# Kernel tuning notes

Hardware: AMD Instinct MI355X
Metric: run time of the kernel (lower is better)

The kernel has to match this reference:

```python
import jax, jax.numpy as jnp
import numpy as np

B, D_IN, C, P = 8192, 2048, 1000, 256


def setup_inputs() -> dict:
    key = jax.random.key(0)
    ks = jax.random.split(key, 6)
    return {
        "x": jax.random.normal(ks[0], (B, D_IN), dtype=jnp.float32),
        "Wm": jax.random.normal(ks[1], (C, D_IN), dtype=jnp.float32) * (1.0 / np.sqrt(D_IN)),
        "bm": jax.random.normal(ks[2], (C,), dtype=jnp.float32) * 0.01,
        "u": jax.random.normal(ks[3], (P, C), dtype=jnp.float32),
        "v": jax.random.normal(ks[4], (P, C), dtype=jnp.float32),
        "w": jax.random.normal(ks[5], (P, 1), dtype=jnp.float32),
    }


def reference(x, Wm, bm, u, v, w):
    # Backbone: Linear(D_IN -> C) producing per-instance logits (B, C)
    preds = jnp.einsum("bd,cd->bc", x, Wm) + bm
    # Gated attention, fully batched (replaces per-instance Python loop):
    # tanh(u @ pred) * sigmoid(v @ pred)  -> (B, P)
    gated = jnp.tanh(jnp.einsum("bc,pc->bp", preds, u)) * jax.nn.sigmoid(
        jnp.einsum("bc,pc->bp", preds, v)
    )
    scores = (gated @ w).ravel()          # (B,)
    attention = jax.nn.softmax(scores)    # softmax over instances
    total_pred = jnp.sum(preds * attention[:, None])
    return preds, total_pred
```

## Files before the change

### kernel.cpp

```cpp
#include <hip/hip_runtime.h>
#include <hip/hip_fp16.h>

typedef _Float16 half8 __attribute__((ext_vector_type(8)));
typedef float f32x4 __attribute__((ext_vector_type(4)));

#define B_   8192
#define DIN  2048
#define C_   1000
#define CP   1024
#define NP2  512

static const size_t OFF_XH  = 0;
static const size_t OFF_WH  = OFF_XH  + (size_t)B_ * DIN * 2;
static const size_t OFF_UVH = OFF_WH  + (size_t)CP * DIN * 2;
static const size_t OFF_PH  = OFF_UVH + (size_t)NP2 * CP * 2;
static const size_t OFF_SC  = OFF_PH  + (size_t)B_ * CP * 2;
static const size_t OFF_RS  = OFF_SC  + (size_t)B_ * 4;
static const size_t WS_NEED = OFF_RS  + (size_t)B_ * 4;

__device__ __forceinline__ void gload16(const void* g, void* l) {
  __builtin_amdgcn_global_load_lds(
      (const __attribute__((address_space(1))) void*)g,
      (__attribute__((address_space(3))) void*)l, 16, 0, 0);
}

__global__ __launch_bounds__(256) void prep_kernel(
    const float* __restrict__ x, const float* __restrict__ Wm,
    const float* __restrict__ u, const float* __restrict__ v,
    _Float16* __restrict__ xh, _Float16* __restrict__ wh,
    _Float16* __restrict__ uvh, float* __restrict__ scores,
    float* __restrict__ rowsum)
{
  const long NX  = (long)B_ * DIN / 8;
  const long NW  = (long)CP * DIN / 8;
  const long NUV = (long)NP2 * CP / 8;
  const long NZ  = 2 * (long)B_ / 8;
  const long T   = NX + NW + NUV + NZ;
  for (long idx = (long)blockIdx.x * blockDim.x + threadIdx.x; idx < T;
       idx += (long)gridDim.x * blockDim.x) {
    if (idx < NX) {
      long e = idx * 8;
      float4 p0 = *(const float4*)(x + e);
      float4 p1 = *(const float4*)(x + e + 4);
      half8 h;
      h[0] = (_Float16)p0.x; h[1] = (_Float16)p0.y; h[2] = (_Float16)p0.z; h[3] = (_Float16)p0.w;
      h[4] = (_Float16)p1.x; h[5] = (_Float16)p1.y; h[6] = (_Float16)p1.z; h[7] = (_Float16)p1.w;
      *(half8*)(xh + e) = h;
    } else if (idx < NX + NW) {
      long e = (idx - NX) * 8;
      int row = (int)(e >> 11);
      half8 h;
      if (row < C_) {
        float4 p0 = *(const float4*)(Wm + e);
        float4 p1 = *(const float4*)(Wm + e + 4);
        h[0] = (_Float16)p0.x; h[1] = (_Float16)p0.y; h[2] = (_Float16)p0.z; h[3] = (_Float16)p0.w;
        h[4] = (_Float16)p1.x; h[5] = (_Float16)p1.y; h[6] = (_Float16)p1.z; h[7] = (_Float16)p1.w;
      } else {
        h = (half8)(_Float16)0.f;
      }
      *(half8*)(wh + e) = h;
    } else if (idx < NX + NW + NUV) {
      long e = (idx - NX - NW) * 8;
      int j = (int)(e >> 10);
      int k = (int)(e & 1023);
      const float* src = (j & 1) ? v : u;
      int p = j >> 1;
      half8 h;
      #pragma unroll
      for (int t = 0; t < 8; ++t) {
        int kk = k + t;
        h[t] = (kk < C_) ? (_Float16)src[(size_t)p * C_ + kk] : (_Float16)0.f;
      }
      *(half8*)(uvh + e) = h;
    } else {
      long e = (idx - NX - NW - NUV) * 8;
      float4 z = {0.f, 0.f, 0.f, 0.f};
      if (e < B_) {
        *(float4*)(scores + e) = z; *(float4*)(scores + e + 4) = z;
      } else {
        long r = e - B_;
        *(float4*)(rowsum + r) = z; *(float4*)(rowsum + r + 4) = z;
      }
    }
  }
}

__global__ __launch_bounds__(512) void gemm1_kernel(
    const _Float16* __restrict__ xh, const _Float16* __restrict__ wh,
    const float* __restrict__ bmv, float* __restrict__ preds,
    _Float16* __restrict__ predsh, float* __restrict__ rowsum)
{
  __shared__ _Float16 lds[3 * 24576];
  const int tid  = threadIdx.x;
  const int lane = tid & 63;
  const int w    = tid >> 6;
  const int wm   = w >> 2;
  const int wn   = w & 3;
  const int bm0  = blockIdx.x * 256;
  const int bn0  = blockIdx.y * 128;

  f32x4 acc[8][2] = {};

  const _Float16* srcA[4];
  const _Float16* srcB[2];
  #pragma unroll
  for (int k = 0; k < 4; ++k) {
    int slot = k * 512 + tid;
    int row  = slot >> 3;
    int cb   = (slot & 7) << 4;
    int scb  = cb ^ ((row & 7) << 4);
    srcA[k] = xh + (size_t)(bm0 + row) * DIN + (scb >> 1);
  }
  #pragma unroll
  for (int k = 0; k < 2; ++k) {
    int slot = k * 512 + tid;
    int row  = slot >> 3;
    int cb   = (slot & 7) << 4;
    int scb  = cb ^ ((row & 7) << 4);
    srcB[k] = wh + (size_t)(bn0 + row) * DIN + (scb >> 1);
  }

  int aoff[8][2], boff[2][2];
  #pragma unroll
  for (int m = 0; m < 8; ++m) {
    #pragma unroll
    for (int ks = 0; ks < 2; ++ks) {
      int ra = wm * 128 + m * 16 + (lane & 15);
      int kb = ks * 64 + (lane >> 4) * 16;
      aoff[m][ks] = ra * 128 + (kb ^ ((ra & 7) << 4));
    }
  }
  #pragma unroll
  for (int n = 0; n < 2; ++n) {
    #pragma unroll
    for (int ks = 0; ks < 2; ++ks) {
      int rb = wn * 32 + n * 16 + (lane & 15);
      int kb = ks * 64 + (lane >> 4) * 16;
      boff[n][ks] = 32768 + rb * 128 + (kb ^ ((rb & 7) << 4));
    }
  }

  auto stageSet = [&](int b, int which) {
    char* base = (char*)lds + b * 49152;
    if (which < 4) gload16(srcA[which], base + which * 8192 + w * 1024);
    else           gload16(srcB[which - 4], base + 32768 + (which - 4) * 8192 + w * 1024);
  };
  auto advance = [&]() {
    #pragma unroll
    for (int k = 0; k < 4; ++k) srcA[k] += 64;
    #pragma unroll
    for (int k = 0; k < 2; ++k) srcB[k] += 64;
  };

  const int NT = DIN / 64;

  #pragma unroll
  for (int q = 0; q < 6; ++q) stageSet(0, q);
  advance();
  #pragma unroll
  for (int q = 0; q < 6; ++q) stageSet(1, q);
  advance();
  asm volatile("s_waitcnt vmcnt(6)" ::: "memory");
  __builtin_amdgcn_s_barrier();
  asm volatile("" ::: "memory");

  int c = 0;
  #pragma unroll 1
  for (int t = 0; t < NT; ++t) {
    const char* bufc = (const char*)lds + c * 49152;
    int sb = c - 1; if (sb < 0) sb = 2;
    const bool st = (t + 2 < NT);

    half8 a2[4][2], b2[2][2];
    #pragma unroll
    for (int m = 0; m < 4; ++m)
      #pragma unroll
      for (int ks = 0; ks < 2; ++ks)
        a2[m][ks] = *(const half8*)(bufc + aoff[m][ks]);
    #pragma unroll
    for (int n = 0; n < 2; ++n)
      #pragma unroll
      for (int ks = 0; ks < 2; ++ks)
        b2[n][ks] = *(const half8*)(bufc + boff[n][ks]);
    if (st) { stageSet(sb, 0); stageSet(sb, 1); stageSet(sb, 2); }
    __builtin_amdgcn_s_barrier();
    asm volatile("" ::: "memory");
    __builtin_amdgcn_s_setprio(1);
    #pragma unroll
    for (int m = 0; m < 4; ++m)
      #pragma unroll
      for (int n = 0; n < 2; ++n)
        #pragma unroll
        for (int ks = 0; ks < 2; ++ks)
          acc[m][n] = __builtin_amdgcn_mfma_f32_16x16x32_f16(a2[m][ks], b2[n][ks], acc[m][n], 0, 0, 0);
    __builtin_amdgcn_s_setprio(0);
    __builtin_amdgcn_s_barrier();
    asm volatile("" ::: "memory");

    #pragma unroll
    for (int m = 0; m < 4; ++m)
      #pragma unroll
      for (int ks = 0; ks < 2; ++ks)
        a2[m][ks] = *(const half8*)(bufc + aoff[m + 4][ks]);
    if (st) { stageSet(sb, 3); stageSet(sb, 4); stageSet(sb, 5); advance(); }
    __builtin_amdgcn_s_barrier();
    asm volatile("" ::: "memory");
    __builtin_amdgcn_s_setprio(1);
    #pragma unroll
    for (int m = 0; m < 4; ++m)
      #pragma unroll
      for (int n = 0; n < 2; ++n)
        #pragma unroll
        for (int ks = 0; ks < 2; ++ks)
          acc[m + 4][n] = __builtin_amdgcn_mfma_f32_16x16x32_f16(a2[m][ks], b2[n][ks], acc[m + 4][n], 0, 0, 0);
    __builtin_amdgcn_s_setprio(0);
    if (st)                 asm volatile("s_waitcnt vmcnt(6)" ::: "memory");
    else if (t + 1 < NT)    asm volatile("s_waitcnt vmcnt(0)" ::: "memory");
    __builtin_amdgcn_s_barrier();
    asm volatile("" ::: "memory");

    c = (c == 2) ? 0 : c + 1;
  }

  float rp[8][4] = {};
  #pragma unroll
  for (int m = 0; m < 8; ++m) {
    #pragma unroll
    for (int n = 0; n < 2; ++n) {
      f32x4 d = acc[m][n];
      int gc = bn0 + wn * 32 + n * 16 + (lane & 15);
      float bias = (gc < C_) ? bmv[gc] : 0.f;
      #pragma unroll
      for (int j = 0; j < 4; ++j) {
        int gr = bm0 + wm * 128 + m * 16 + (lane >> 4) * 4 + j;
        float val = d[j] + bias;
        predsh[(size_t)gr * CP + gc] = (_Float16)val;
        if (gc < C_) preds[(size_t)gr * C_ + gc] = val;
        rp[m][j] += val;
      }
    }
  }
  #pragma unroll
  for (int m = 0; m < 8; ++m) {
    #pragma unroll
    for (int j = 0; j < 4; ++j) {
      float s = rp[m][j];
      s += __shfl_xor(s, 1); s += __shfl_xor(s, 2);
      s += __shfl_xor(s, 4); s += __shfl_xor(s, 8);
      if ((lane & 15) == 0) {
        int gr = bm0 + wm * 128 + m * 16 + (lane >> 4) * 4 + j;
        atomicAdd(&rowsum[gr], s);
      }
    }
  }
}

__global__ __launch_bounds__(256) void gemm2_kernel(
    const _Float16* __restrict__ predsh, const _Float16* __restrict__ uvh,
    const float* __restrict__ wv, float* __restrict__ scores)
{
  __shared__ _Float16 sA[2][64 * 64];
  __shared__ _Float16 sB[2][128 * 64];
  const int tid  = threadIdx.x;
  const int lane = tid & 63;
  const int w    = tid >> 6;
  const int wm   = w >> 1, wn = w & 1;
  const int bm0  = blockIdx.x * 64;
  const int bn0  = blockIdx.y * 128;

  f32x4 acc[2][4] = {};

  const _Float16* srcA[2]; const _Float16* srcB[4];
  #pragma unroll
  for (int i = 0; i < 2; ++i) {
    int slot = i * 256 + tid;
    int row  = slot >> 3;
    int cb   = (slot & 7) << 4;
    int scb  = cb ^ ((row & 7) << 4);
    srcA[i] = predsh + (size_t)(bm0 + row) * CP + (scb >> 1);
  }
  #pragma unroll
  for (int i = 0; i < 4; ++i) {
    int slot = i * 256 + tid;
    int row  = slot >> 3;
    int cb   = (slot & 7) << 4;
    int scb  = cb ^ ((row & 7) << 4);
    srcB[i] = uvh + (size_t)(bn0 + row) * CP + (scb >> 1);
  }
  int aoff[2][2], boff[4][2];
  #pragma unroll
  for (int ks = 0; ks < 2; ++ks) {
    int kb = ks * 64 + (lane >> 4) * 16;
    #pragma unroll
    for (int mi = 0; mi < 2; ++mi) {
      int ra = wm * 32 + mi * 16 + (lane & 15);
      aoff[mi][ks] = ra * 128 + (kb ^ ((ra & 7) << 4));
    }
    #pragma unroll
    for (int ni = 0; ni < 4; ++ni) {
      int rb = wn * 64 + ni * 16 + (lane & 15);
      boff[ni][ks] = rb * 128 + (kb ^ ((rb & 7) << 4));
    }
  }

  auto stage = [&](int c) {
    #pragma unroll
    for (int i = 0; i < 2; ++i) {
      gload16(srcA[i], &sA[c][(i * 4 + w) * 512]);
      srcA[i] += 64;
    }
    #pragma unroll
    for (int i = 0; i < 4; ++i) {
      gload16(srcB[i], &sB[c][(i * 4 + w) * 512]);
      srcB[i] += 64;
    }
  };

  auto compute = [&](int c) {
    const char* bA = (const char*)&sA[c][0];
    const char* bB = (const char*)&sB[c][0];
    #pragma unroll
    for (int ks = 0; ks < 2; ++ks) {
      half8 a[2], b[4];
      #pragma unroll
      for (int mi = 0; mi < 2; ++mi) a[mi] = *(const half8*)(bA + aoff[mi][ks]);
      #pragma unroll
      for (int ni = 0; ni < 4; ++ni) b[ni] = *(const half8*)(bB + boff[ni][ks]);
      #pragma unroll
      for (int mi = 0; mi < 2; ++mi)
        #pragma unroll
        for (int ni = 0; ni < 4; ++ni)
          acc[mi][ni] = __builtin_amdgcn_mfma_f32_16x16x32_f16(a[mi], b[ni], acc[mi][ni], 0, 0, 0);
    }
  };

  const int NT = CP / 64;
  stage(0);
  #pragma unroll 1
  for (int kt = 0; kt < NT; kt += 2) {
    stage(1);
    asm volatile("s_waitcnt vmcnt(6)" ::: "memory");
    __builtin_amdgcn_s_barrier();
    asm volatile("" ::: "memory");
    compute(0);
    __builtin_amdgcn_s_barrier();
    asm volatile("" ::: "memory");
    if (kt + 2 < NT) {
      stage(0);
      asm volatile("s_waitcnt vmcnt(6)" ::: "memory");
    } else {
      asm volatile("s_waitcnt vmcnt(0)" ::: "memory");
    }
    __builtin_amdgcn_s_barrier();
    asm volatile("" ::: "memory");
    compute(1);
    __builtin_amdgcn_s_barrier();
    asm volatile("" ::: "memory");
  }

  float sp[2][4] = {};
  #pragma unroll
  for (int mi = 0; mi < 2; ++mi) {
    #pragma unroll
    for (int ni = 0; ni < 4; ++ni) {
      f32x4 d = acc[mi][ni];
      int gc = bn0 + wn * 64 + ni * 16 + (lane & 15);
      float wq = wv[gc >> 1];
      bool even = ((gc & 1) == 0);
      #pragma unroll
      for (int j = 0; j < 4; ++j) {
        float t  = d[j];
        float pr = __shfl_xor(t, 1);
        float th = 2.f / (1.f + __expf(-2.f * t)) - 1.f;
        float sg = 1.f / (1.f + __expf(-pr));
        sp[mi][j] += even ? (th * sg * wq) : 0.f;
      }
    }
  }
  #pragma unroll
  for (int mi = 0; mi < 2; ++mi) {
    #pragma unroll
    for (int j = 0; j < 4; ++j) {
      float s = sp[mi][j];
      s += __shfl_xor(s, 1); s += __shfl_xor(s, 2);
      s += __shfl_xor(s, 4); s += __shfl_xor(s, 8);
      if ((lane & 15) == 0) {
        int gr = bm0 + wm * 32 + mi * 16 + (lane >> 4) * 4 + j;
        atomicAdd(&scores[gr], s);
      }
    }
  }
}

__global__ __launch_bounds__(1024) void final_kernel(
    const float* __restrict__ scores, const float* __restrict__ rowsum,
    float* __restrict__ out)
{
  __shared__ float red[16], red2[16];
  const int t = threadIdx.x;
  const int lane = t & 63, wid = t >> 6;
  float s[8];
  float m = -3.4e38f;
  #pragma unroll
  for (int i = 0; i < 8; ++i) { s[i] = scores[t + i * 1024]; m = fmaxf(m, s[i]); }
  #pragma unroll
  for (int off = 1; off < 64; off <<= 1) m = fmaxf(m, __shfl_xor(m, off));
  if (lane == 0) red[wid] = m;
  __syncthreads();
  #pragma unroll
  for (int i = 0; i < 16; ++i) m = fmaxf(m, red[i]);
  __syncthreads();

  float se = 0.f, sr = 0.f;
  #pragma unroll
  for (int i = 0; i < 8; ++i) {
    float e = __expf(s[i] - m);
    se += e;
    sr += e * rowsum[t + i * 1024];
  }
  #pragma unroll
  for (int off = 1; off < 64; off <<= 1) { se += __shfl_xor(se, off); sr += __shfl_xor(sr, off); }
  if (lane == 0) { red[wid] = se; red2[wid] = sr; }
  __syncthreads();
  if (t == 0) {
    float tse = 0.f, tsr = 0.f;
    for (int i = 0; i < 16; ++i) { tse += red[i]; tsr += red2[i]; }
    out[0] = tsr / tse;
  }
}

extern "C" void kernel_launch(void* const* d_in, const int* in_sizes, int n_in,
                              void* d_out, int out_size, void* d_ws, size_t ws_size,
                              hipStream_t stream)
{
  const float* x   = (const float*)d_in[0];
  const float* Wm  = (const float*)d_in[1];
  const float* bmv = (const float*)d_in[2];
  const float* u   = (const float*)d_in[3];
  const float* v   = (const float*)d_in[4];
  const float* wv  = (const float*)d_in[5];
  float* out = (float*)d_out;

  if (ws_size < WS_NEED) return;

  char* ws = (char*)d_ws;
  _Float16* xh     = (_Float16*)(ws + OFF_XH);
  _Float16* wh     = (_Float16*)(ws + OFF_WH);
  _Float16* uvh    = (_Float16*)(ws + OFF_UVH);
  _Float16* predsh = (_Float16*)(ws + OFF_PH);
  float*    scores = (float*)(ws + OFF_SC);
  float*    rowsum = (float*)(ws + OFF_RS);

  prep_kernel<<<2048, 256, 0, stream>>>(x, Wm, u, v, xh, wh, uvh, scores, rowsum);
  gemm1_kernel<<<dim3(32, 8), 512, 0, stream>>>(xh, wh, bmv, out, predsh, rowsum);
  gemm2_kernel<<<dim3(128, 4), 256, 0, stream>>>(predsh, uvh, wv, scores);
  final_kernel<<<1, 1024, 0, stream>>>(scores, rowsum, out + (size_t)B_ * C_);
}
```

Baseline: 96.04 us.

## Reshape gemm1 warp tiling to 4x4 and software-pipeline LDS fragment reads across quadrants

```diff
diff --git a/kernel.cpp b/kernel.cpp
--- a/kernel.cpp
+++ b/kernel.cpp
@@ -17,6 +17,9 @@
 static const size_t OFF_SC  = OFF_PH  + (size_t)B_ * CP * 2;
 static const size_t OFF_RS  = OFF_SC  + (size_t)B_ * 4;
 static const size_t WS_NEED = OFF_RS  + (size_t)B_ * 4;
+
+#define FENCE asm volatile("" ::: "memory")
+#define BARRIER do { FENCE; __builtin_amdgcn_s_barrier(); FENCE; } while (0)
 
 __device__ __forceinline__ void gload16(const void* g, void* l) {
   __builtin_amdgcn_global_load_lds(
@@ -94,12 +97,12 @@
   const int tid  = threadIdx.x;
   const int lane = tid & 63;
   const int w    = tid >> 6;
-  const int wm   = w >> 2;
-  const int wn   = w & 3;
+  const int wm   = w >> 1;
+  const int wn   = w & 1;
   const int bm0  = blockIdx.x * 256;
   const int bn0  = blockIdx.y * 128;
 
-  f32x4 acc[8][2] = {};
+  f32x4 acc[4][4] = {};
 
   const _Float16* srcA[4];
   const _Float16* srcB[2];
@@ -120,119 +123,194 @@
     srcB[k] = wh + (size_t)(bn0 + row) * DIN + (scb >> 1);
   }
 
-  int aoff[8][2], boff[2][2];
-  #pragma unroll
-  for (int m = 0; m < 8; ++m) {
+  int aoff[4][2], boff[4][2];
+  #pragma unroll
+  for (int m = 0; m < 4; ++m) {
     #pragma unroll
     for (int ks = 0; ks < 2; ++ks) {
-      int ra = wm * 128 + m * 16 + (lane & 15);
+      int ra = wm * 64 + m * 16 + (lane & 15);
       int kb = ks * 64 + (lane >> 4) * 16;
       aoff[m][ks] = ra * 128 + (kb ^ ((ra & 7) << 4));
     }
   }
   #pragma unroll
-  for (int n = 0; n < 2; ++n) {
+  for (int n = 0; n < 4; ++n) {
     #pragma unroll
     for (int ks = 0; ks < 2; ++ks) {
-      int rb = wn * 32 + n * 16 + (lane & 15);
+      int rb = wn * 64 + n * 16 + (lane & 15);
       int kb = ks * 64 + (lane >> 4) * 16;
       boff[n][ks] = 32768 + rb * 128 + (kb ^ ((rb & 7) << 4));
     }
   }
 
-  auto stageSet = [&](int b, int which) {
-    char* base = (char*)lds + b * 49152;
-    if (which < 4) gload16(srcA[which], base + which * 8192 + w * 1024);
-    else           gload16(srcB[which - 4], base + 32768 + (which - 4) * 8192 + w * 1024);
+  half8 aLa[2][2], aLb[2][2], aHf[2][2], bLf[2][2], bHf[2][2];
+
+  auto stA = [&](int cs, int k) {
+    gload16(srcA[k], (char*)lds + cs * 49152 + k * 8192 + w * 1024);
+  };
+  auto stB = [&](int cs, int k) {
+    gload16(srcB[k], (char*)lds + cs * 49152 + 32768 + k * 8192 + w * 1024);
   };
   auto advance = [&]() {
     #pragma unroll
     for (int k = 0; k < 4; ++k) srcA[k] += 64;
-    #pragma unroll
-    for (int k = 0; k < 2; ++k) srcB[k] += 64;
-  };
-
-  const int NT = DIN / 64;
-
-  #pragma unroll
-  for (int q = 0; q < 6; ++q) stageSet(0, q);
-  advance();
-  #pragma unroll
-  for (int q = 0; q < 6; ++q) stageSet(1, q);
-  advance();
-  asm volatile("s_waitcnt vmcnt(6)" ::: "memory");
-  __builtin_amdgcn_s_barrier();
-  asm volatile("" ::: "memory");
-
-  int c = 0;
-  #pragma unroll 1
-  for (int t = 0; t < NT; ++t) {
-    const char* bufc = (const char*)lds + c * 49152;
-    int sb = c - 1; if (sb < 0) sb = 2;
-    const bool st = (t + 2 < NT);
-
-    half8 a2[4][2], b2[2][2];
-    #pragma unroll
-    for (int m = 0; m < 4; ++m)
+    srcB[0] += 64; srcB[1] += 64;
+  };
+  auto rdAH = [&](const char* b) {
+    #pragma unroll
+    for (int m = 0; m < 2; ++m)
       #pragma unroll
       for (int ks = 0; ks < 2; ++ks)
-        a2[m][ks] = *(const half8*)(bufc + aoff[m][ks]);
+        aHf[m][ks] = *(const half8*)(b + aoff[m + 2][ks]);
+  };
+  auto rdBH = [&](const char* b) {
     #pragma unroll
     for (int n = 0; n < 2; ++n)
       #pragma unroll
       for (int ks = 0; ks < 2; ++ks)
-        b2[n][ks] = *(const half8*)(bufc + boff[n][ks]);
-    if (st) { stageSet(sb, 0); stageSet(sb, 1); stageSet(sb, 2); }
-    __builtin_amdgcn_s_barrier();
-    asm volatile("" ::: "memory");
-    __builtin_amdgcn_s_setprio(1);
-    #pragma unroll
-    for (int m = 0; m < 4; ++m)
+        bHf[n][ks] = *(const half8*)(b + boff[n + 2][ks]);
+  };
+  auto rdAL = [&](const char* b, half8 (&d)[2][2]) {
+    #pragma unroll
+    for (int m = 0; m < 2; ++m)
+      #pragma unroll
+      for (int ks = 0; ks < 2; ++ks)
+        d[m][ks] = *(const half8*)(b + aoff[m][ks]);
+  };
+  auto rdBL = [&](const char* b) {
+    #pragma unroll
+    for (int n = 0; n < 2; ++n)
+      #pragma unroll
+      for (int ks = 0; ks < 2; ++ks)
+        bLf[n][ks] = *(const half8*)(b + boff[n][ks]);
+  };
+  auto mfLL = [&](half8 (&aL)[2][2]) {
+    #pragma unroll
+    for (int m = 0; m < 2; ++m)
       #pragma unroll
       for (int n = 0; n < 2; ++n)
         #pragma unroll
         for (int ks = 0; ks < 2; ++ks)
-          acc[m][n] = __builtin_amdgcn_mfma_f32_16x16x32_f16(a2[m][ks], b2[n][ks], acc[m][n], 0, 0, 0);
-    __builtin_amdgcn_s_setprio(0);
-    __builtin_amdgcn_s_barrier();
-    asm volatile("" ::: "memory");
-
-    #pragma unroll
-    for (int m = 0; m < 4; ++m)
-      #pragma unroll
-      for (int ks = 0; ks < 2; ++ks)
-        a2[m][ks] = *(const half8*)(bufc + aoff[m + 4][ks]);
-    if (st) { stageSet(sb, 3); stageSet(sb, 4); stageSet(sb, 5); advance(); }
-    __builtin_amdgcn_s_barrier();
-    asm volatile("" ::: "memory");
-    __builtin_amdgcn_s_setprio(1);
-    #pragma unroll
-    for (int m = 0; m < 4; ++m)
+          acc[m][n] = __builtin_amdgcn_mfma_f32_16x16x32_f16(aL[m][ks], bLf[n][ks], acc[m][n], 0, 0, 0);
+  };
+  auto mfHL = [&]() {
+    #pragma unroll
+    for (int m = 0; m < 2; ++m)
       #pragma unroll
       for (int n = 0; n < 2; ++n)
         #pragma unroll
         for (int ks = 0; ks < 2; ++ks)
-          acc[m + 4][n] = __builtin_amdgcn_mfma_f32_16x16x32_f16(a2[m][ks], b2[n][ks], acc[m + 4][n], 0, 0, 0);
-    __builtin_amdgcn_s_setprio(0);
-    if (st)                 asm volatile("s_waitcnt vmcnt(6)" ::: "memory");
-    else if (t + 1 < NT)    asm volatile("s_waitcnt vmcnt(0)" ::: "memory");
-    __builtin_amdgcn_s_barrier();
-    asm volatile("" ::: "memory");
-
-    c = (c == 2) ? 0 : c + 1;
-  }
-
-  float rp[8][4] = {};
-  #pragma unroll
-  for (int m = 0; m < 8; ++m) {
-    #pragma unroll
-    for (int n = 0; n < 2; ++n) {
+          acc[m + 2][n] = __builtin_amdgcn_mfma_f32_16x16x32_f16(aHf[m][ks], bLf[n][ks], acc[m + 2][n], 0, 0, 0);
+  };
+  auto mfLH = [&](half8 (&aL)[2][2]) {
+    #pragma unroll
+    for (int m = 0; m < 2; ++m)
+      #pragma unroll
+      for (int n = 0; n < 2; ++n)
+        #pragma unroll
+        for (int ks = 0; ks < 2; ++ks)
+          acc[m][n + 2] = __builtin_amdgcn_mfma_f32_16x16x32_f16(aL[m][ks], bHf[n][ks], acc[m][n + 2], 0, 0, 0);
+  };
+  auto mfHH = [&]() {
+    #pragma unroll
+    for (int m = 0; m < 2; ++m)
+      #pragma unroll
+      for (int n = 0; n < 2; ++n)
+        #pragma unroll
+        for (int ks = 0; ks < 2; ++ks)
+          acc[m + 2][n + 2] = __builtin_amdgcn_mfma_f32_16x16x32_f16(aHf[m][ks], bHf[n][ks], acc[m + 2][n + 2], 0, 0, 0);
+  };
+
+  #pragma unroll
+  for (int k = 0; k < 4; ++k) stA(0, k);
+  stB(0, 0); stB(0, 1);
+  advance();
+  #pragma unroll
+  for (int k = 0; k < 4; ++k) stA(1, k);
+  stB(1, 0); stB(1, 1);
+  advance();
+  asm volatile("s_waitcnt vmcnt(6)" ::: "memory");
+  BARRIER;
+  rdAL((const char*)lds, aLa);
+  rdBL((const char*)lds);
+
+  int c0 = 0;
+  #pragma unroll 1
+  for (int t = 0; t < 30; t += 2) {
+    const int c1 = (c0 == 2) ? 0 : c0 + 1;
+    const int c2 = (c1 == 2) ? 0 : c1 + 1;
+    const char* bt  = (const char*)lds + c0 * 49152;
+    const char* bn1 = (const char*)lds + c1 * 49152;
+    const char* bn2 = (const char*)lds + c2 * 49152;
+
+    rdAH(bt);  stA(c2, 0); stA(c2, 1);
+    BARRIER;
+    __builtin_amdgcn_s_setprio(1); mfLL(aLa); __builtin_amdgcn_s_setprio(0);
+
+    rdBH(bt);  stA(c2, 2); stA(c2, 3);
+    asm volatile("s_waitcnt vmcnt(4)" ::: "memory");
+    BARRIER;
+    __builtin_amdgcn_s_setprio(1); mfHL(); __builtin_amdgcn_s_setprio(0);
+
+    rdAL(bn1, aLb);  stB(c2, 0);
+    BARRIER;
+    __builtin_amdgcn_s_setprio(1); mfLH(aLa); __builtin_amdgcn_s_setprio(0);
+
+    rdBL(bn1);  stB(c2, 1); advance();
+    BARRIER;
+    __builtin_amdgcn_s_setprio(1); mfHH(); __builtin_amdgcn_s_setprio(0);
+
+    rdAH(bn1);  stA(c0, 0); stA(c0, 1);
+    BARRIER;
+    __builtin_amdgcn_s_setprio(1); mfLL(aLb); __builtin_amdgcn_s_setprio(0);
+
+    rdBH(bn1);  stA(c0, 2); stA(c0, 3);
+    asm volatile("s_waitcnt vmcnt(4)" ::: "memory");
+    BARRIER;
+    __builtin_amdgcn_s_setprio(1); mfHL(); __builtin_amdgcn_s_setprio(0);
+
+    rdAL(bn2, aLa);  stB(c0, 0);
+    BARRIER;
+    __builtin_amdgcn_s_setprio(1); mfLH(aLb); __builtin_amdgcn_s_setprio(0);
+
+    rdBL(bn2);  stB(c0, 1); advance();
+    BARRIER;
+    __builtin_amdgcn_s_setprio(1); mfHH(); __builtin_amdgcn_s_setprio(0);
+
+    c0 = c2;
+  }
+
+  {
+    const char* bt  = (const char*)lds;
+    const char* bn1 = (const char*)lds + 49152;
+    rdAH(bt);
+    BARRIER;
+    __builtin_amdgcn_s_setprio(1); mfLL(aLa); __builtin_amdgcn_s_setprio(0);
+    rdBH(bt);
+    asm volatile("s_waitcnt vmcnt(0)" ::: "memory");
+    BARRIER;
+    __builtin_amdgcn_s_setprio(1); mfHL(); __builtin_amdgcn_s_setprio(0);
+    rdAL(bn1, aLb);
+    BARRIER;
+    __builtin_amdgcn_s_setprio(1); mfLH(aLa); __builtin_amdgcn_s_setprio(0);
+    rdBL(bn1);
+    BARRIER;
+    __builtin_amdgcn_s_setprio(1); mfHH(); __builtin_amdgcn_s_setprio(0);
+    rdAH(bn1); rdBH(bn1);
+    mfLL(aLb); mfHL(); mfLH(aLb); mfHH();
+  }
+
+  float rp[4][4] = {};
+  #pragma unroll
+  for (int m = 0; m < 4; ++m) {
+    #pragma unroll
+    for (int n = 0; n < 4; ++n) {
       f32x4 d = acc[m][n];
-      int gc = bn0 + wn * 32 + n * 16 + (lane & 15);
+      int gc = bn0 + wn * 64 + n * 16 + (lane & 15);
       float bias = (gc < C_) ? bmv[gc] : 0.f;
       #pragma unroll
       for (int j = 0; j < 4; ++j) {
-        int gr = bm0 + wm * 128 + m * 16 + (lane >> 4) * 4 + j;
+        int gr = bm0 + wm * 64 + m * 16 + (lane >> 4) * 4 + j;
         float val = d[j] + bias;
         predsh[(size_t)gr * CP + gc] = (_Float16)val;
         if (gc < C_) preds[(size_t)gr * C_ + gc] = val;
@@ -241,14 +319,14 @@
     }
   }
   #pragma unroll
-  for (int m = 0; m < 8; ++m) {
+  for (int m = 0; m < 4; ++m) {
     #pragma unroll
     for (int j = 0; j < 4; ++j) {
       float s = rp[m][j];
       s += __shfl_xor(s, 1); s += __shfl_xor(s, 2);
       s += __shfl_xor(s, 4); s += __shfl_xor(s, 8);
       if ((lane & 15) == 0) {
-        int gr = bm0 + wm * 128 + m * 16 + (lane >> 4) * 4 + j;
+        int gr = bm0 + wm * 64 + m * 16 + (lane >> 4) * 4 + j;
         atomicAdd(&rowsum[gr], s);
       }
     }
@@ -340,22 +418,18 @@
   for (int kt = 0; kt < NT; kt += 2) {
     stage(1);
     asm volatile("s_waitcnt vmcnt(6)" ::: "memory");
-    __builtin_amdgcn_s_barrier();
-    asm volatile("" ::: "memory");
+    BARRIER;
     compute(0);
-    __builtin_amdgcn_s_barrier();
-    asm volatile("" ::: "memory");
+    BARRIER;
     if (kt + 2 < NT) {
       stage(0);
       asm volatile("s_waitcnt vmcnt(6)" ::: "memory");
     } else {
       asm volatile("s_waitcnt vmcnt(0)" ::: "memory");
     }
-    __builtin_amdgcn_s_barrier();
-    asm volatile("" ::: "memory");
+    BARRIER;
     compute(1);
-    __builtin_amdgcn_s_barrier();
-    asm volatile("" ::: "memory");
+    BARRIER;
   }
 
   float sp[2][4] = {};
```

Result: faster. 90.41 us (-5.9%).
